# Optimization experiments

Hardware: AMD Instinct MI355X
Metric: run time of the kernel (lower is better)

Reference implementation:

```python
import jax, jax.numpy as jnp
import numpy as np

B, L, D, N = 4, 1024, 1024, 16
HD = D // N
DFF = 4 * D
EPS = 1e-5


def _ln(x, g, b):
    m = jnp.mean(x, axis=-1, keepdims=True)
    v = jnp.mean(jnp.square(x - m), axis=-1, keepdims=True)
    return (x - m) * jax.lax.rsqrt(v + EPS) * g + b


def setup_inputs() -> dict:
    key = jax.random.key(0)
    ks = jax.random.split(key, 8)
    s = 0.02
    return {
        "x": jax.random.normal(ks[0], (B, L, D), jnp.float32),
        "decay": jax.random.uniform(ks[1], (N, L, L), jnp.float32),
        "ln1_g": jnp.ones((D,), jnp.float32),
        "ln1_b": jnp.zeros((D,), jnp.float32),
        "proj_W": jax.random.normal(ks[2], (4 * D, D), jnp.float32) * s,
        "proj_b": jnp.zeros((4 * D,), jnp.float32),
        "reto_W": jax.random.normal(ks[3], (D, D), jnp.float32) * s,
        "reto_b": jnp.zeros((D,), jnp.float32),
        "ln2_g": jnp.ones((D,), jnp.float32),
        "ln2_b": jnp.zeros((D,), jnp.float32),
        "ffn1_W": jax.random.normal(ks[4], (DFF, D), jnp.float32) * s,
        "ffn1_b": jnp.zeros((DFF,), jnp.float32),
        "ffn2_W": jax.random.normal(ks[5], (D, DFF), jnp.float32) * s,
        "ffn2_b": jnp.zeros((D,), jnp.float32),
    }


def reference(x, decay, ln1_g, ln1_b, proj_W, proj_b, reto_W, reto_b,
              ln2_g, ln2_b, ffn1_W, ffn1_b, ffn2_W, ffn2_b):
    ln_x = _ln(x, ln1_g, ln1_b)
    p = ln_x @ proj_W.T + proj_b                      # [B, L, 4D]
    q, k, v, xo = jnp.split(p, 4, axis=-1)            # each [B, L, D]

    def heads(t):  # [B, L, D] -> [B, N, L, HD]
        return t.reshape(B, L, N, HD).transpose(0, 2, 1, 3)

    q, k, v = heads(q), heads(k), heads(v)
    scores = jnp.einsum('bnld,bnmd->bnlm', q, k) * decay[None]  # [B,N,L,L]
    ret = jnp.einsum('bnlm,bnmd->bnld', scores, v)              # [B,N,L,HD]
    ret = ret.transpose(0, 2, 1, 3).reshape(B, L, D)
    ret = ret * jax.nn.silu(xo)                                  # gated
    ret = ret @ reto_W.T + reto_b
    x = x + ret
    h = _ln(x, ln2_g, ln2_b)
    h = jax.nn.gelu(h @ ffn1_W.T + ffn1_b, approximate=False) @ ffn2_W.T + ffn2_b
    return x + h
```

## Files before the change

kernel.cpp:

```cpp
#include <hip/hip_runtime.h>


typedef _Float16 f16;
typedef _Float16 f16x8 __attribute__((ext_vector_type(8)));
typedef float floatx4 __attribute__((ext_vector_type(4)));

#define EP_BIAS_F16      0
#define EP_DECAY_F16     1
#define EP_BIAS_GELU_F16 2
#define EP_PARTIAL_F32   3

template <bool F32> struct out_sel { typedef f16 T; };
template <> struct out_sel<true>   { typedef float T; };

__device__ __forceinline__ void gload_lds16(const void* g, void* s) {
    __builtin_amdgcn_global_load_lds(
        (const __attribute__((address_space(1))) unsigned int*)g,
        (__attribute__((address_space(3))) unsigned int*)s, 16, 0, 0);
}

__device__ __forceinline__ float erf_fast(float x) {
    const float ax = fabsf(x);
    const float t  = __builtin_amdgcn_rcpf(1.f + 0.3275911f * ax);
    const float p  = t * (0.254829592f + t * (-0.284496736f + t * (1.421413741f +
                     t * (-1.453152027f + t * 1.061405429f))));
    const float r  = 1.f - p * __expf(-ax * ax);
    return copysignf(r, x);
}

__global__ __launch_bounds__(256, 2) void attn_fused(
    const f16* __restrict__ p, const f16* __restrict__ vT,
    const float* __restrict__ decay, f16* __restrict__ gated)
{
    const int y  = blockIdx.y;
    const int bp = y >> 4, h = y & 15;
    const int m0 = blockIdx.x * 64;

    __shared__ __align__(16) f16 Kb[2][64 * 64];
    __shared__ __align__(16) f16 Vb[2][64 * 64];
    __shared__ __align__(16) f16 Ss[4][16 * 68];

    const int t    = threadIdx.x;
    const int lane = t & 63;
    const int w    = t >> 6;
    const int quad = lane >> 4;
    const int fr   = lane & 15;
    const int wq0  = w * 16;

    const int b0 = bp * 2, b1 = b0 + 1;
    const f16*   Qg0 = p + (size_t)(b0 * 1024 + m0) * 4096 + h * 64;
    const f16*   Qg1 = p + (size_t)(b1 * 1024 + m0) * 4096 + h * 64;
    const f16*   Kg0 = p + (size_t)(b0 * 1024) * 4096 + 1024 + h * 64;
    const f16*   Kg1 = p + (size_t)(b1 * 1024) * 4096 + 1024 + h * 64;
    const f16*   Vg0 = vT + (size_t)(b0 * 16 + h) * 65536;
    const f16*   Vg1 = vT + (size_t)(b1 * 16 + h) * 65536;
    const f16*   XOg0 = p + (size_t)(b0 * 1024 + m0) * 4096 + 3072 + h * 64;
    const f16*   XOg1 = p + (size_t)(b1 * 1024 + m0) * 4096 + 3072 + h * 64;
    const float* Dg  = decay + (size_t)h * 1048576 + (size_t)m0 * 1024;

    f16x8 q00, q01, q10, q11;
    {
        const size_t qrow = (size_t)(wq0 + fr) * 4096;
        q00 = *(const f16x8*)(Qg0 + qrow + (0 * 4 + quad) * 8);
        q01 = *(const f16x8*)(Qg0 + qrow + (1 * 4 + quad) * 8);
        q10 = *(const f16x8*)(Qg1 + qrow + (0 * 4 + quad) * 8);
        q11 = *(const f16x8*)(Qg1 + qrow + (1 * 4 + quad) * 8);
    }

    floatx4 oa0[4] = {}, oa1[4] = {};
    float dA[16], dB[16];

    const float* Dt = Dg + (size_t)(wq0 + quad * 4) * 1024 + fr;

#define DLOAD(dst, jj) { _Pragma("unroll") \
    for (int tn = 0; tn < 4; ++tn) { _Pragma("unroll") \
      for (int r = 0; r < 4; ++r) \
        dst[tn * 4 + r] = Dt[(size_t)r * 1024 + (jj) + tn * 16]; } }

#define STAGE(Kgp, Vgp, jj, pb) { _Pragma("unroll") \
    for (int i = 0; i < 2; ++i) { \
      const int ci = t + i * 256; \
      const int r  = ci >> 3; \
      const int c  = ((ci & 7) ^ (r & 7)) * 8; \
      gload_lds16((Kgp) + (size_t)((jj) + r) * 4096 + c, &Kb[pb][ci * 8]); \
      gload_lds16((Vgp) + (size_t)r * 1024 + (jj) + c, &Vb[pb][ci * 8]); \
    } }

#define STEP(qa, qb, oa, dreg, pb) { \
    floatx4 sa[4] = {}; \
    _Pragma("unroll") \
    for (int kc = 0; kc < 2; ++kc) { \
      const int cc = kc * 4 + quad; \
      f16x8 bf[4]; \
      _Pragma("unroll") \
      for (int tn = 0; tn < 4; ++tn) { \
        const int kv = tn * 16 + fr; \
        bf[tn] = *(const f16x8*)&Kb[pb][(kv * 8 + (cc ^ (kv & 7))) * 8]; \
      } \
      _Pragma("unroll") \
      for (int tn = 0; tn < 4; ++tn) \
        sa[tn] = __builtin_amdgcn_mfma_f32_16x16x32_f16(kc ? (qb) : (qa), bf[tn], sa[tn], 0, 0, 0); \
    } \
    _Pragma("unroll") \
    for (int tn = 0; tn < 4; ++tn) { _Pragma("unroll") \
      for (int r = 0; r < 4; ++r) \
        Ss[w][(quad * 4 + r) * 68 + tn * 16 + fr] = (f16)(sa[tn][r] * dreg[tn * 4 + r]); } \
    _Pragma("unroll") \
    for (int kc = 0; kc < 2; ++kc) { \
      const int cc = kc * 4 + quad; \
      const f16x8 af = *(const f16x8*)&Ss[w][fr * 68 + cc * 8]; \
      f16x8 bf[4]; \
      _Pragma("unroll") \
      for (int tn = 0; tn < 4; ++tn) { \
        const int d = tn * 16 + fr; \
        bf[tn] = *(const f16x8*)&Vb[pb][(d * 8 + (cc ^ (d & 7))) * 8]; \
      } \
      _Pragma("unroll") \
      for (int tn = 0; tn < 4; ++tn) \
        oa[tn] = __builtin_amdgcn_mfma_f32_16x16x32_f16(af, bf[tn], oa[tn], 0, 0, 0); \
    } }

#define EPILOG(oa, XOgp, bq) { \
    _Pragma("unroll") \
    for (int tn = 0; tn < 4; ++tn) { _Pragma("unroll") \
      for (int r = 0; r < 4; ++r) { \
        const int qrow = wq0 + quad * 4 + r; \
        const int d = tn * 16 + fr; \
        float g = (float)XOgp[(size_t)qrow * 4096 + d]; \
        g = g * __builtin_amdgcn_rcpf(1.f + __expf(-g)); \
        Ss[w][(quad * 4 + r) * 68 + tn * 16 + fr] = (f16)(oa[tn][r] * g); \
      } } \
    f16* Og = gated + (size_t)((bq) * 1024 + m0 + wq0) * 1024 + h * 64; \
    _Pragma("unroll") \
    for (int i = 0; i < 2; ++i) { \
      const int jj = lane + i * 64; \
      const int rr = jj >> 3; \
      const int cc = jj & 7; \
      const uint2 lo = *(const uint2*)&Ss[w][rr * 68 + cc * 8]; \
      const uint2 hi = *(const uint2*)&Ss[w][rr * 68 + cc * 8 + 4]; \
      uint4 val = make_uint4(lo.x, lo.y, hi.x, hi.y); \
      *(uint4*)(Og + (size_t)rr * 1024 + cc * 8) = val; \
    } }

    STAGE(Kg0, Vg0, 0, 0);
    DLOAD(dA, 0);
    __syncthreads();

    for (int tt = 0; tt < 16; tt += 2) {
        const int j0 = tt << 6;
        STAGE(Kg1, Vg1, j0, 1);
        STEP(q00, q01, oa0, dA, 0);
        __syncthreads();
        STAGE(Kg0, Vg0, j0 + 64, 0);
        DLOAD(dB, j0 + 64);
        STEP(q10, q11, oa1, dA, 1);
        __syncthreads();
        STAGE(Kg1, Vg1, j0 + 64, 1);
        STEP(q00, q01, oa0, dB, 0);
        __syncthreads();
        if (tt < 14) {
            STAGE(Kg0, Vg0, j0 + 128, 0);
            DLOAD(dA, j0 + 128);
        }
        STEP(q10, q11, oa1, dB, 1);
        __syncthreads();
    }

    EPILOG(oa0, XOg0, b0);
    EPILOG(oa1, XOg1, b1);

#undef DLOAD
#undef STAGE
#undef STEP
#undef EPILOG
}

template <int BM, int BN, int WM, int WN, int EP, int XSWZ>
__global__ __launch_bounds__(256, 4) void gemm_bt(
    const f16* __restrict__ A, const f16* __restrict__ B, void* __restrict__ Cv,
    int M, int N, int K, int lda, int ldb, int ldc,
    long long sAo, long long sAi, long long sBo, long long sBi,
    long long sCo, long long sCi, int inner,
    int nsplit, int Kc, long long sCk,
    const float* __restrict__ bias,
    const void* __restrict__ aux, long long sXo, long long sXi, int ldaux)
{
    constexpr bool OUT_F32 = (EP == EP_PARTIAL_F32);
    typedef typename out_sel<OUT_F32>::T OutT;
    constexpr int ESIZE       = OUT_F32 ? 4 : 2;
    constexpr int CSTRIDE     = BN + 4;
    constexpr int TILE_BYTES  = (BM + BN) * 64 * 2;
    constexpr int STAGE_BYTES = OUT_F32 ? 0 : BM * CSTRIDE * ESIZE;
    constexpr int SMEM_BYTES  = TILE_BYTES > STAGE_BYTES ? TILE_BYTES : STAGE_BYTES;

    __shared__ __align__(16) char smem[SMEM_BYTES];
    f16*  As = (f16*)smem;
    f16*  Bs = (f16*)(smem + BM * 128);
    OutT* Cs = (OutT*)smem;

    int z = blockIdx.z;
    const int ks = z % nsplit; z /= nsplit;
    const int zo = z / inner, zi = z % inner;
    A += zo * sAo + zi * sAi;
    B += zo * sBo + zi * sBi;
    const long long cOff = (long long)zo * sCo + (long long)zi * sCi + (long long)ks * sCk;
    const long long xOff = (long long)zo * sXo + (long long)zi * sXi;

    int bx = blockIdx.x, by = blockIdx.y;
    if constexpr (XSWZ) {
        const int gx  = gridDim.x;
        const int nb  = gx * gridDim.y;
        const int lin = bx + gx * by;
        const int nlin = (lin & 7) * (nb >> 3) + (lin >> 3);
        bx = nlin % gx;
        by = nlin / gx;
    }
    const int m0 = by * BM;
    const int n0 = bx * BN;

    const int t    = threadIdx.x;
    const int lane = t & 63;
    const int w    = t >> 6;
    const int wm   = (w >> 1) * (WM * 16);
    const int wn   = (w & 1) * (WN * 16);
    const int fr   = lane & 15;
    const int quad = lane >> 4;

    constexpr int ACH = BM / 32;
    constexpr int BCH = BN / 32;

    floatx4 acc[WM][WN] = {};

    const int kbeg = ks * Kc, kend = kbeg + Kc;
    for (int kk = kbeg; kk < kend; kk += 64) {
#pragma unroll
        for (int i = 0; i < ACH; ++i) {
            const int ci = t + i * 256;
            const int r  = ci >> 3;
            const int c  = ((ci & 7) ^ (r & 7)) * 8;
            gload_lds16(A + (size_t)(m0 + r) * lda + kk + c, &As[ci * 8]);
        }
#pragma unroll
        for (int i = 0; i < BCH; ++i) {
            const int ci = t + i * 256;
            const int r  = ci >> 3;
            const int c  = ((ci & 7) ^ (r & 7)) * 8;
            gload_lds16(B + (size_t)(n0 + r) * ldb + kk + c, &Bs[ci * 8]);
        }
        __syncthreads();

#pragma unroll
        for (int kh = 0; kh < 2; ++kh) {
            const int cc = kh * 4 + quad;
            f16x8 af[WM], bf[WN];
#pragma unroll
            for (int tm = 0; tm < WM; ++tm) {
                const int r = wm + tm * 16 + fr;
                af[tm] = *(const f16x8*)&As[(r * 8 + (cc ^ (r & 7))) * 8];
            }
#pragma unroll
            for (int tn = 0; tn < WN; ++tn) {
                const int r = wn + tn * 16 + fr;
                bf[tn] = *(const f16x8*)&Bs[(r * 8 + (cc ^ (r & 7))) * 8];
            }
#pragma unroll
            for (int tm = 0; tm < WM; ++tm)
#pragma unroll
                for (int tn = 0; tn < WN; ++tn)
                    acc[tm][tn] = __builtin_amdgcn_mfma_f32_16x16x32_f16(af[tm], bf[tn], acc[tm][tn], 0, 0, 0);
        }
        __syncthreads();
    }

    const int er = quad * 4;
    const int ec = lane & 15;
    if constexpr (OUT_F32) {
        float* Pg = (float*)Cv + cOff;
#pragma unroll
        for (int tm = 0; tm < WM; ++tm)
#pragma unroll
            for (int tn = 0; tn < WN; ++tn)
#pragma unroll
                for (int r = 0; r < 4; ++r) {
                    const int grow = m0 + wm + tm * 16 + er + r;
                    const int gcol = n0 + wn + tn * 16 + ec;
                    Pg[(size_t)grow * ldc + gcol] = acc[tm][tn][r];
                }
        return;
    }

#pragma unroll
    for (int tm = 0; tm < WM; ++tm) {
#pragma unroll
        for (int tn = 0; tn < WN; ++tn) {
#pragma unroll
            for (int r = 0; r < 4; ++r) {
                const int lrow = wm + tm * 16 + er + r;
                const int col  = wn + tn * 16 + ec;
                const int grow = m0 + lrow;
                const int gcol = n0 + col;
                const float v = acc[tm][tn][r];
                float val;
                if constexpr (EP == EP_BIAS_F16) {
                    val = v + bias[gcol];
                } else if constexpr (EP == EP_DECAY_F16) {
                    const float* dk = (const float*)aux + xOff;
                    val = v * dk[(size_t)grow * ldaux + gcol];
                } else if constexpr (EP == EP_BIAS_GELU_F16) {
                    const float u = v + bias[gcol];
                    val = 0.5f * u * (1.f + erf_fast(u * 0.70710678118f));
                } else {
                    val = v;
                }
                Cs[lrow * CSTRIDE + col] = (OutT)val;
            }
        }
    }
    __syncthreads();

    constexpr int PER_ROW = BN * ESIZE / 16;
    constexpr int NCHUNK  = (BM * PER_ROW) / 256;
#pragma unroll
    for (int i = 0; i < NCHUNK; ++i) {
        const int j  = t + i * 256;
        const int rr = j / PER_ROW;
        const int cc = j - rr * PER_ROW;
        const char* src = smem + (size_t)rr * (CSTRIDE * ESIZE) + (size_t)cc * 16;
        const uint2 lo = *(const uint2*)src;
        const uint2 hi = *(const uint2*)(src + 8);
        uint4 val = make_uint4(lo.x, lo.y, hi.x, hi.y);
        char* dst = (char*)Cv +
            (size_t)(cOff + (long long)(m0 + rr) * ldc + n0) * ESIZE +
            (size_t)cc * 16;
        *(uint4*)dst = val;
    }
}

__global__ __launch_bounds__(256) void reduce2_bias_res(
    const float4* __restrict__ P, const float* __restrict__ bias,
    const float4* __restrict__ res, float4* __restrict__ out)
{
    const int i = blockIdx.x * 256 + threadIdx.x;
    const int col4 = i & 255;
    const float4 a = P[i];
    const float4 b = P[i + 1048576];
    const float4 r = res[i];
    const float4 bi = ((const float4*)bias)[col4];
    float4 o;
    o.x = a.x + b.x + r.x + bi.x;
    o.y = a.y + b.y + r.y + bi.y;
    o.z = a.z + b.z + r.z + bi.z;
    o.w = a.w + b.w + r.w + bi.w;
    out[i] = o;
}

__global__ __launch_bounds__(256) void ln_to_f16(
    const float* __restrict__ x, const float* __restrict__ g,
    const float* __restrict__ b, f16* __restrict__ out)
{
    const int row = blockIdx.x;
    const int t = threadIdx.x;
    const float4 xv = ((const float4*)(x + (size_t)row * 1024))[t];
    float s  = xv.x + xv.y + xv.z + xv.w;
    float ss = xv.x * xv.x + xv.y * xv.y + xv.z * xv.z + xv.w * xv.w;
    for (int o = 32; o > 0; o >>= 1) {
        s  += __shfl_down(s, o, 64);
        ss += __shfl_down(ss, o, 64);
    }
    __shared__ float red[8];
    const int wv = t >> 6;
    if ((t & 63) == 0) { red[wv] = s; red[wv + 4] = ss; }
    __syncthreads();
    s  = red[0] + red[1] + red[2] + red[3];
    ss = red[4] + red[5] + red[6] + red[7];
    const float mean = s * (1.f / 1024.f);
    const float var  = ss * (1.f / 1024.f) - mean * mean;
    const float rstd = rsqrtf(var + 1e-5f);
    const float4 gv = ((const float4*)g)[t];
    const float4 bv = ((const float4*)b)[t];
    alignas(8) f16 h[4];
    h[0] = (f16)((xv.x - mean) * rstd * gv.x + bv.x);
    h[1] = (f16)((xv.y - mean) * rstd * gv.y + bv.y);
    h[2] = (f16)((xv.z - mean) * rstd * gv.z + bv.z);
    h[3] = (f16)((xv.w - mean) * rstd * gv.w + bv.w);
    ((uint2*)(out + (size_t)row * 1024))[t] = *(uint2*)h;
}

__global__ __launch_bounds__(256) void cast_f32_f16(
    const float* __restrict__ in, f16* __restrict__ out, int n4)
{
    const int i = blockIdx.x * 256 + threadIdx.x;
    if (i < n4) {
        const float4 v = ((const float4*)in)[i];
        alignas(8) f16 h[4] = {(f16)v.x, (f16)v.y, (f16)v.z, (f16)v.w};
        ((uint2*)out)[i] = *(uint2*)h;
    }
}

__global__ __launch_bounds__(256) void transpose_v(
    const f16* __restrict__ p, f16* __restrict__ vT)
{
    const int z = blockIdx.y;
    const int b = z >> 4, h = z & 15;
    const int m0 = blockIdx.x * 64;
    __shared__ f16 tile[64][72];
    const int t = threadIdx.x;
    const f16* src = p + (size_t)(b * 1024 + m0) * 4096 + 2048 + h * 64;
#pragma unroll
    for (int pass = 0; pass < 4; ++pass) {
        const int r = (t >> 4) + pass * 16;
        const int c = (t & 15) * 4;
        *(uint2*)&tile[r][c] = *(const uint2*)(src + (size_t)r * 4096 + c);
    }
    __syncthreads();
    f16* dst = vT + (size_t)z * 65536 + m0;
#pragma unroll
    for (int pass = 0; pass < 4; ++pass) {
        const int d  = (t >> 4) + pass * 16;
        const int mc = (t & 15) * 4;
        alignas(8) f16 tmp[4] = {tile[mc][d], tile[mc + 1][d], tile[mc + 2][d], tile[mc + 3][d]};
        *(uint2*)(dst + (size_t)d * 1024 + mc) = *(uint2*)tmp;
    }
}

extern "C" void kernel_launch(void* const* d_in, const int* in_sizes, int n_in,
                              void* d_out, int out_size, void* d_ws, size_t ws_size,
                              hipStream_t stream) {
    const float* x      = (const float*)d_in[0];
    const float* decay  = (const float*)d_in[1];
    const float* ln1_g  = (const float*)d_in[2];
    const float* ln1_b  = (const float*)d_in[3];
    const float* proj_W = (const float*)d_in[4];
    const float* proj_b = (const float*)d_in[5];
    const float* reto_W = (const float*)d_in[6];
    const float* reto_b = (const float*)d_in[7];
    const float* ln2_g  = (const float*)d_in[8];
    const float* ln2_b  = (const float*)d_in[9];
    const float* ffn1_W = (const float*)d_in[10];
    const float* ffn1_b = (const float*)d_in[11];
    const float* ffn2_W = (const float*)d_in[12];
    const float* ffn2_b = (const float*)d_in[13];
    float* out = (float*)d_out;

    char* w = (char*)d_ws;
    auto alloc = [&](size_t bytes) { char* r = w; w += (bytes + 255) & ~(size_t)255; return r; };
    f16*   Wp   = (f16*)alloc((size_t)4096 * 1024 * 2);
    f16*   Wr   = (f16*)alloc((size_t)1024 * 1024 * 2);
    f16*   W1   = (f16*)alloc((size_t)4096 * 1024 * 2);
    f16*   W2   = (f16*)alloc((size_t)1024 * 4096 * 2);
    f16*   buf8 = (f16*)alloc((size_t)4096 * 1024 * 2);
    f16*   p    = (f16*)alloc((size_t)4096 * 4096 * 2);
    f16*   S    = (f16*)alloc((size_t)16 * 1024 * 1024 * 2);
    float* y    = (float*)alloc((size_t)4096 * 1024 * 4);

    f16*   lnx   = buf8;
    f16*   vT    = buf8;
    f16*   hln   = buf8;
    f16*   gated = Wp;
    f16*   ffh   = p;
    float* Pk    = (float*)S;

    cast_f32_f16<<<4096, 256, 0, stream>>>(proj_W, Wp, 1048576);
    cast_f32_f16<<<1024, 256, 0, stream>>>(reto_W, Wr, 262144);
    cast_f32_f16<<<4096, 256, 0, stream>>>(ffn1_W, W1, 1048576);
    cast_f32_f16<<<4096, 256, 0, stream>>>(ffn2_W, W2, 1048576);

    ln_to_f16<<<4096, 256, 0, stream>>>(x, ln1_g, ln1_b, lnx);

    gemm_bt<128, 128, 4, 4, EP_BIAS_F16, 0><<<dim3(32, 32, 1), 256, 0, stream>>>(
        lnx, Wp, p, 4096, 4096, 1024, 1024, 1024, 4096,
        0, 0, 0, 0, 0, 0, 1, 1, 1024, 0, proj_b, nullptr, 0, 0, 0);

    transpose_v<<<dim3(16, 64), 256, 0, stream>>>(p, vT);

    attn_fused<<<dim3(16, 32), 256, 0, stream>>>(p, vT, decay, gated);

    gemm_bt<128, 128, 4, 4, EP_PARTIAL_F32, 1><<<dim3(8, 32, 2), 256, 0, stream>>>(
        gated, Wr, Pk, 4096, 1024, 1024, 1024, 1024, 1024,
        0, 0, 0, 0, 0, 0, 1, 2, 512, 4194304, nullptr, nullptr, 0, 0, 0);
    reduce2_bias_res<<<4096, 256, 0, stream>>>(
        (const float4*)Pk, reto_b, (const float4*)x, (float4*)y);

    ln_to_f16<<<4096, 256, 0, stream>>>(y, ln2_g, ln2_b, hln);

    gemm_bt<128, 128, 4, 4, EP_BIAS_GELU_F16, 0><<<dim3(32, 32, 1), 256, 0, stream>>>(
        hln, W1, ffh, 4096, 4096, 1024, 1024, 1024, 4096,
        0, 0, 0, 0, 0, 0, 1, 1, 1024, 0, ffn1_b, nullptr, 0, 0, 0);

    gemm_bt<128, 128, 4, 4, EP_PARTIAL_F32, 1><<<dim3(8, 32, 2), 256, 0, stream>>>(
        ffh, W2, Pk, 4096, 1024, 4096, 4096, 4096, 1024,
        0, 0, 0, 0, 0, 0, 1, 2, 2048, 4194304, nullptr, nullptr, 0, 0, 0);
    reduce2_bias_res<<<4096, 256, 0, stream>>>(
        (const float4*)Pk, ffn2_b, (const float4*)y, (float4*)out);
}
```

Baseline: 399.7 us.

## Double attention block to 512 threads with 4-deep K/V ring and vmcnt barriers

The attention kernel now runs 512 threads per block covering 128 query rows, so each staged K/V tile is shared by twice as many waves and the grid is halved. The double-buffered LDS is replaced by a four-slot ring with two loads in flight, and __syncthreads is replaced by explicit s_waitcnt vmcnt(2) plus barrier so prefetches overlap compute. LDS use doubles, which may limit occupancy, and the hand-tuned wait counts are fragile.

```diff
diff --git a/kernel.cpp b/kernel.cpp
--- a/kernel.cpp
+++ b/kernel.cpp
@@ -28,17 +28,17 @@
     return copysignf(r, x);
 }
 
-__global__ __launch_bounds__(256, 2) void attn_fused(
+__global__ __launch_bounds__(512, 2) void attn_fused(
     const f16* __restrict__ p, const f16* __restrict__ vT,
     const float* __restrict__ decay, f16* __restrict__ gated)
 {
     const int y  = blockIdx.y;
     const int bp = y >> 4, h = y & 15;
-    const int m0 = blockIdx.x * 64;
-
-    __shared__ __align__(16) f16 Kb[2][64 * 64];
-    __shared__ __align__(16) f16 Vb[2][64 * 64];
-    __shared__ __align__(16) f16 Ss[4][16 * 68];
+    const int m0 = blockIdx.x * 128;
+
+    __shared__ __align__(16) f16 Kb[4][64 * 64];
+    __shared__ __align__(16) f16 Vb[4][64 * 64];
+    __shared__ __align__(16) f16 Ss[8][16 * 68];
 
     const int t    = threadIdx.x;
     const int lane = t & 63;
@@ -77,14 +77,14 @@
       for (int r = 0; r < 4; ++r) \
         dst[tn * 4 + r] = Dt[(size_t)r * 1024 + (jj) + tn * 16]; } }
 
-#define STAGE(Kgp, Vgp, jj, pb) { _Pragma("unroll") \
-    for (int i = 0; i < 2; ++i) { \
-      const int ci = t + i * 256; \
-      const int r  = ci >> 3; \
-      const int c  = ((ci & 7) ^ (r & 7)) * 8; \
-      gload_lds16((Kgp) + (size_t)((jj) + r) * 4096 + c, &Kb[pb][ci * 8]); \
-      gload_lds16((Vgp) + (size_t)r * 1024 + (jj) + c, &Vb[pb][ci * 8]); \
-    } }
+#define STAGE(Kgp, Vgp, jj, pb) { \
+    const int r_ = t >> 3; \
+    const int c_ = ((t & 7) ^ (r_ & 7)) * 8; \
+    gload_lds16((Kgp) + (size_t)((jj) + r_) * 4096 + c_, &Kb[pb][t * 8]); \
+    gload_lds16((Vgp) + (size_t)r_ * 1024 + (jj) + c_, &Vb[pb][t * 8]); }
+
+#define VMBAR(N) { asm volatile("s_waitcnt vmcnt(" #N ")" ::: "memory"); \
+    __builtin_amdgcn_s_barrier(); __builtin_amdgcn_sched_barrier(0); }
 
 #define STEP(qa, qb, oa, dreg, pb) { \
     floatx4 sa[4] = {}; \
@@ -144,26 +144,38 @@
 
     STAGE(Kg0, Vg0, 0, 0);
     DLOAD(dA, 0);
-    __syncthreads();
-
-    for (int tt = 0; tt < 16; tt += 2) {
-        const int j0 = tt << 6;
-        STAGE(Kg1, Vg1, j0, 1);
+    STAGE(Kg1, Vg1, 0, 1);
+    VMBAR(2);
+
+    for (int i = 0; i < 7; ++i) {
+        const int j1 = i * 128 + 64;
+        const int j2 = i * 128 + 128;
+        STAGE(Kg0, Vg0, j1, 2);
+        DLOAD(dB, j1);
         STEP(q00, q01, oa0, dA, 0);
-        __syncthreads();
-        STAGE(Kg0, Vg0, j0 + 64, 0);
-        DLOAD(dB, j0 + 64);
+        VMBAR(2);
+        STAGE(Kg1, Vg1, j1, 3);
         STEP(q10, q11, oa1, dA, 1);
-        __syncthreads();
-        STAGE(Kg1, Vg1, j0 + 64, 1);
-        STEP(q00, q01, oa0, dB, 0);
-        __syncthreads();
-        if (tt < 14) {
-            STAGE(Kg0, Vg0, j0 + 128, 0);
-            DLOAD(dA, j0 + 128);
-        }
-        STEP(q10, q11, oa1, dB, 1);
-        __syncthreads();
+        VMBAR(2);
+        STAGE(Kg0, Vg0, j2, 0);
+        DLOAD(dA, j2);
+        STEP(q00, q01, oa0, dB, 2);
+        VMBAR(2);
+        STAGE(Kg1, Vg1, j2, 1);
+        STEP(q10, q11, oa1, dB, 3);
+        VMBAR(2);
+    }
+    {
+        STAGE(Kg0, Vg0, 960, 2);
+        DLOAD(dB, 960);
+        STEP(q00, q01, oa0, dA, 0);
+        VMBAR(2);
+        STAGE(Kg1, Vg1, 960, 3);
+        STEP(q10, q11, oa1, dA, 1);
+        VMBAR(2);
+        STEP(q00, q01, oa0, dB, 2);
+        VMBAR(0);
+        STEP(q10, q11, oa1, dB, 3);
     }
 
     EPILOG(oa0, XOg0, b0);
@@ -171,6 +183,7 @@
 
 #undef DLOAD
 #undef STAGE
+#undef VMBAR
 #undef STEP
 #undef EPILOG
 }
@@ -473,7 +486,7 @@
 
     transpose_v<<<dim3(16, 64), 256, 0, stream>>>(p, vT);
 
-    attn_fused<<<dim3(16, 32), 256, 0, stream>>>(p, vT, decay, gated);
+    attn_fused<<<dim3(8, 32), 512, 0, stream>>>(p, vT, decay, gated);
 
     gemm_bt<128, 128, 4, 4, EP_PARTIAL_F32, 1><<<dim3(8, 32, 2), 256, 0, stream>>>(
         gated, Wr, Pk, 4096, 1024, 1024, 1024, 1024, 1024,
```

New measurement: 392.7 us. No clear change (-1.7%).
